# Performance work log

Hardware: AMD Instinct MI355X
Metric: run time of the kernel (lower is better)

## Reference

```python
import jax, jax.numpy as jnp
import numpy as np

NUM_BINS = 256          # CLAHE histogram bins (kornia default)
GRID = (8, 8)           # CLAHE tile grid (kornia default)
LOG_GAIN = 2.5          # module init arg
CLIP_LIMIT = 1.0        # module init arg


def normalize_in_range(x, lo=0.0, hi=1.0):
    mn = x.min()
    mx = x.max()
    return (x - mn) / (mx - mn) * (hi - lo) + lo


def adjust_log(x, gain):
    # skimage/kornia log adjust: gain * log2(1 + x)
    return gain * jnp.log2(1.0 + x)


def equalize_clahe(x, clip_limit=CLIP_LIMIT, grid=GRID):
    B, C, H, W = x.shape
    gh, gw = grid
    th = -(-H // gh)   # ceil tile height
    tw = -(-W // gw)   # ceil tile width
    Hp, Wp = th * gh, tw * gw
    if (Hp, Wp) != (H, W):
        x = jnp.pad(x, ((0, 0), (0, 0), (0, Hp - H), (0, Wp - W)), mode='reflect')

    # bin index per pixel (values saturated into [0,1])
    xc = jnp.clip(x, 0.0, 1.0)
    bins = jnp.clip((xc * NUM_BINS).astype(jnp.int32), 0, NUM_BINS - 1)  # B,C,Hp,Wp

    # --- per-tile histograms: (B*C*gh*gw) tiles of th*tw pixels ---
    tb = bins.reshape(B, C, gh, th, gw, tw).transpose(0, 1, 2, 4, 3, 5)
    tb = tb.reshape(B * C * gh * gw, th * tw)
    hist = jax.vmap(lambda ix: jnp.bincount(ix, length=NUM_BINS))(tb).astype(jnp.float32)

    pixels = th * tw
    # --- clip + uniform redistribution of excess ---
    if clip_limit > 0:
        clip_max = max(int(clip_limit * pixels // NUM_BINS), 1)
        excess = jnp.maximum(hist - clip_max, 0.0).sum(-1)
        hist = jnp.minimum(hist, float(clip_max))
        redist = jnp.floor(excess / NUM_BINS)
        residual = excess - redist * NUM_BINS
        hist = hist + redist[:, None] \
             + (jnp.arange(NUM_BINS)[None, :] < residual[:, None]).astype(hist.dtype)

    # --- CDF -> LUT in [0, 255] ---
    lut = jnp.clip(jnp.floor(jnp.cumsum(hist, -1) * ((NUM_BINS - 1) / pixels)), 0.0, NUM_BINS - 1.0)
    lut = lut.reshape(B, C, gh, gw, NUM_BINS)

    # --- bilinear interpolation between the 4 neighboring tile LUTs ---
    iy = jnp.arange(Hp, dtype=jnp.float32)
    ty = (iy + 0.5) / th - 0.5
    y0f = jnp.floor(ty)
    wy = (ty - y0f)[:, None]                                   # Hp x 1
    y0 = jnp.clip(y0f.astype(jnp.int32), 0, gh - 1)[:, None]
    y1 = jnp.clip(y0f.astype(jnp.int32) + 1, 0, gh - 1)[:, None]

    ix = jnp.arange(Wp, dtype=jnp.float32)
    tx = (ix + 0.5) / tw - 0.5
    x0f = jnp.floor(tx)
    wx = (tx - x0f)[None, :]
    x0 = jnp.clip(x0f.astype(jnp.int32), 0, gw - 1)[None, :]
    x1 = jnp.clip(x0f.astype(jnp.int32) + 1, 0, gw - 1)[None, :]

    flat_lut = lut.reshape(-1)
    bidx = jnp.arange(B)[:, None, None, None]
    cidx = jnp.arange(C)[None, :, None, None]

    def gather(yi, xi):
        idx = (((bidx * C + cidx) * gh + yi) * gw + xi) * NUM_BINS + bins
        return flat_lut[idx]

    v = (1.0 - wy) * ((1.0 - wx) * gather(y0, x0) + wx * gather(y0, x1)) \
        + wy * ((1.0 - wx) * gather(y1, x0) + wx * gather(y1, x1))
    out = v / (NUM_BINS - 1)
    return out[..., :H, :W]


def setup_inputs() -> dict:
    key = jax.random.key(0)
    x = jax.random.uniform(key, (8, 1, 2048, 2048), dtype=jnp.float32)
    return {"x": x}


def reference(x):
    shape = x.shape
    x = normalize_in_range(x, 0.0, 1.0)
    x = adjust_log(x, gain=LOG_GAIN)
    x = equalize_clahe(x, clip_limit=CLIP_LIMIT)
    x = normalize_in_range(x, 0.0, 1.0)
    return x.reshape(shape)
```

## Files before the change

### kernel.cpp

```cpp
#include <hip/hip_runtime.h>

#define NIMG 8
#define IMH 2048
#define IMW 2048
#define GH 8
#define GW 8
#define TH 256
#define TW 256
#define NBINS 256
#define NTPI 64
#define CLIP_MAXF 256.0f
#define LUT_SCALE 0.0038909912109375f
#define LOG_GAIN_F 2.5f

#define MM_BLOCKS 1024
#define APPLY_BLOCKS (16 * 16 * NIMG)

__device__ __forceinline__ int pix_bin(float v, float mn, float den) {
    float xn = (v - mn) / den;
    float t  = LOG_GAIN_F * log2f(1.0f + xn);
    float xc = fminf(fmaxf(t, 0.0f), 1.0f);
    int b = (int)(xc * 256.0f);
    return min(max(b, 0), 255);
}

__device__ __forceinline__ void mm4(float4 v, float& mn, float& mx) {
    mn = fminf(mn, fminf(fminf(v.x, v.y), fminf(v.z, v.w)));
    mx = fmaxf(mx, fmaxf(fmaxf(v.x, v.y), fmaxf(v.z, v.w)));
}

template <int NWAVES>
__device__ __forceinline__ void block_minmax(float& mn, float& mx, int t) {
#pragma unroll
    for (int m = 32; m >= 1; m >>= 1) {
        mn = fminf(mn, __shfl_xor(mn, m, 64));
        mx = fmaxf(mx, __shfl_xor(mx, m, 64));
    }
    __shared__ float smn[NWAVES], smx[NWAVES];
    int wid = t >> 6, lid = t & 63;
    if (lid == 0) { smn[wid] = mn; smx[wid] = mx; }
    __syncthreads();
    if (t == 0) {
#pragma unroll
        for (int i = 1; i < NWAVES; i++) { mn = fminf(mn, smn[i]); mx = fmaxf(mx, smx[i]); }
    }
}

__global__ __launch_bounds__(256) void k_minmax_in(const float4* __restrict__ x,
                                                   float2* __restrict__ red) {
    int t = threadIdx.x;
    size_t base = (size_t)blockIdx.x * 8192 + t;
    float mn = 3.4e38f, mx = -3.4e38f;
#pragma unroll
    for (int k = 0; k < 32; k += 4) {
        float4 v0 = x[base + (size_t)(k + 0) * 256];
        float4 v1 = x[base + (size_t)(k + 1) * 256];
        float4 v2 = x[base + (size_t)(k + 2) * 256];
        float4 v3 = x[base + (size_t)(k + 3) * 256];
        mm4(v0, mn, mx); mm4(v1, mn, mx); mm4(v2, mn, mx); mm4(v3, mn, mx);
    }
    block_minmax<4>(mn, mx, t);
    if (t == 0) red[blockIdx.x] = make_float2(mn, mx);
}

__global__ __launch_bounds__(256) void k_reduce_minmax(const float2* __restrict__ red, int n,
                                                       float* __restrict__ sc, int slot) {
    int t = threadIdx.x;
    float mn = 3.4e38f, mx = -3.4e38f;
    for (int i = t; i < n; i += 256) {
        float2 p = red[i];
        mn = fminf(mn, p.x);
        mx = fmaxf(mx, p.y);
    }
    block_minmax<4>(mn, mx, t);
    if (t == 0) { sc[slot] = mn; sc[slot + 1] = mx; }
}

template <bool STOREBINS>
__global__ __launch_bounds__(512) void k_hist(const float* __restrict__ x,
                                              const float* __restrict__ sc,
                                              float* __restrict__ hist,
                                              uchar4* __restrict__ bins) {
    __shared__ unsigned sh[NBINS];
    int t = threadIdx.x;
    if (t < NBINS) sh[t] = 0u;
    __syncthreads();

    int tile = blockIdx.x;
    int img  = blockIdx.y;
    int ty = tile >> 3, tx = tile & 7;
    float mn = sc[0], mx = sc[1];
    float den = mx - mn;

    size_t base = ((size_t)img * IMH + (size_t)ty * TH) * IMW + (size_t)tx * TW;
    const float* xt = x + base;
    int lid = t & 63;
    int rowoff = t >> 6;
    int c4 = t & 63;

    for (int it = 0; it < 32; ++it) {
        int r = (it << 3) + rowoff;
        float4 v = *(const float4*)(xt + (size_t)r * IMW + (c4 << 2));
        int b[4];
        b[0] = pix_bin(v.x, mn, den);
        b[1] = pix_bin(v.y, mn, den);
        b[2] = pix_bin(v.z, mn, den);
        b[3] = pix_bin(v.w, mn, den);
#pragma unroll
        for (int j = 0; j < 4; j++) {
            bool hot = (b[j] == 255);
            unsigned long long m = __ballot(hot);
            if (!hot) atomicAdd(&sh[b[j]], 1u);
            if (lid == 0 && m) atomicAdd(&sh[255], (unsigned)__popcll(m));
        }
        if (STOREBINS) {
            uchar4 q;
            q.x = (unsigned char)b[0]; q.y = (unsigned char)b[1];
            q.z = (unsigned char)b[2]; q.w = (unsigned char)b[3];
            bins[(base + (size_t)r * IMW + (size_t)(c4 << 2)) >> 2] = q;
        }
    }
    __syncthreads();
    if (t < NBINS)
        hist[((size_t)img * NTPI + tile) * NBINS + t] = (float)sh[t];
}

__global__ __launch_bounds__(256) void k_lut(const float* __restrict__ hist,
                                             float* __restrict__ lut) {
    int t = threadIdx.x;
    int tile = blockIdx.x;
    float h = hist[(size_t)tile * NBINS + t];
    float ex = fmaxf(h - CLIP_MAXF, 0.0f);

    float s = ex;
#pragma unroll
    for (int m = 1; m < 64; m <<= 1) s += __shfl_xor(s, m, 64);
    __shared__ float wpart[4];
    int wid = t >> 6, lid = t & 63;
    if (lid == 0) wpart[wid] = s;
    __syncthreads();
    float excess = wpart[0] + wpart[1] + wpart[2] + wpart[3];

    h = fminf(h, CLIP_MAXF);
    float redist   = floorf(excess * (1.0f / 256.0f));
    float residual = excess - redist * 256.0f;
    h = h + redist + (((float)t < residual) ? 1.0f : 0.0f);

    float c = h;
#pragma unroll
    for (int m = 1; m < 64; m <<= 1) {
        float o = __shfl_up(c, m, 64);
        if (lid >= m) c += o;
    }
    __shared__ float wsum[4];
    if (lid == 63) wsum[wid] = c;
    __syncthreads();
    float off = 0.0f;
    for (int i = 0; i < wid; i++) off += wsum[i];
    c += off;

    float l = fminf(floorf(c * LUT_SCALE), 255.0f);
    l = fmaxf(l, 0.0f);
    lut[(size_t)tile * NBINS + t] = l;
}

template <bool USE_BINS, bool FINAL>
__global__ __launch_bounds__(256) void k_apply(const uchar4* __restrict__ bins,
                                               const float* __restrict__ x,
                                               const float* __restrict__ lut,
                                               const float* __restrict__ sc,
                                               float2* __restrict__ red,
                                               float4* __restrict__ out) {
    __shared__ float L[4][NBINS];
    int t = threadIdx.x;
    int qx = blockIdx.x, qy = blockIdx.y, img = blockIdx.z;
    int ty = qy >> 1, tx = qx >> 1;
    int yA = (qy & 1) ? ty : max(ty - 1, 0);
    int yB = (qy & 1) ? min(ty + 1, GH - 1) : ty;
    int xA = (qx & 1) ? tx : max(tx - 1, 0);
    int xB = (qx & 1) ? min(tx + 1, GW - 1) : tx;

    const float* lb = lut + (size_t)img * NTPI * NBINS;
    L[0][t] = lb[(size_t)(yA * GW + xA) * NBINS + t];
    L[1][t] = lb[(size_t)(yA * GW + xB) * NBINS + t];
    L[2][t] = lb[(size_t)(yB * GW + xA) * NBINS + t];
    L[3][t] = lb[(size_t)(yB * GW + xB) * NBINS + t];
    __syncthreads();

    float mn = 0.f, den = 1.f;
    if (!USE_BINS) { mn = sc[0]; den = sc[1] - mn; }
    float pmn = 0.f, oscale = 1.f;
    if (FINAL) {
        float vmn = sc[2], vmx = sc[3];
        pmn = vmn * (1.0f / 255.0f);
        float pmx = vmx * (1.0f / 255.0f);
        oscale = 1.0f / (pmx - pmn);
    }

    float vmnl = 3.4e38f, vmxl = -3.4e38f;
    int gy0 = qy << 7, gx0 = qx << 7;
    int rowoff = t >> 5;
    int c4 = t & 31;

    for (int it = 0; it < 16; ++it) {
        int r = (it << 3) + rowoff;
        int iy = gy0 + r;
        int ix0 = gx0 + (c4 << 2);
        size_t pidx = ((size_t)img * IMH + iy) * IMW + ix0;

        int b[4];
        if (USE_BINS) {
            uchar4 q = bins[pidx >> 2];
            b[0] = q.x; b[1] = q.y; b[2] = q.z; b[3] = q.w;
        } else {
            float4 v = *(const float4*)(x + pidx);
            b[0] = pix_bin(v.x, mn, den);
            b[1] = pix_bin(v.y, mn, den);
            b[2] = pix_bin(v.z, mn, den);
            b[3] = pix_bin(v.w, mn, den);
        }

        float tyf = ((float)iy + 0.5f) * (1.0f / 256.0f) - 0.5f;
        float wy = tyf - floorf(tyf);
        float4 o;
        float* op = &o.x;
#pragma unroll
        for (int j = 0; j < 4; j++) {
            float txf = ((float)(ix0 + j) + 0.5f) * (1.0f / 256.0f) - 0.5f;
            float wx = txf - floorf(txf);
            float g00 = L[0][b[j]], g01 = L[1][b[j]];
            float g10 = L[2][b[j]], g11 = L[3][b[j]];
            float v = (1.0f - wy) * ((1.0f - wx) * g00 + wx * g01) +
                      wy * ((1.0f - wx) * g10 + wx * g11);
            if (FINAL) {
                float p = v * (1.0f / 255.0f);
                op[j] = (p - pmn) * oscale;
            } else {
                vmnl = fminf(vmnl, v);
                vmxl = fmaxf(vmxl, v);
            }
        }
        if (FINAL) out[pidx >> 2] = o;
    }

    if (!FINAL) {
        block_minmax<4>(vmnl, vmxl, t);
        if (t == 0) {
            int bid = (img * 16 + qy) * 16 + qx;
            red[bid] = make_float2(vmnl, vmxl);
        }
    }
}

extern "C" void kernel_launch(void* const* d_in, const int* in_sizes, int n_in,
                              void* d_out, int out_size, void* d_ws, size_t ws_size,
                              hipStream_t stream) {
    const float* x = (const float*)d_in[0];
    float4* out = (float4*)d_out;

    unsigned char* ws = (unsigned char*)d_ws;
    float* sc     = (float*)ws;
    float* hist   = (float*)(ws + 64);
    float* lut    = (float*)(ws + 64 + 512 * 1024);
    float2* red1  = (float2*)(ws + 64 + 1024 * 1024);
    float2* red2  = (float2*)(ws + 64 + 1024 * 1024 + 8192);
    uchar4* bins  = (uchar4*)(ws + 2 * 1024 * 1024);

    size_t need_bins = 2 * 1024 * 1024 + (size_t)NIMG * IMH * IMW;
    bool use_bins = (ws_size >= need_bins);

    k_minmax_in<<<dim3(MM_BLOCKS), dim3(256), 0, stream>>>((const float4*)x, red1);
    k_reduce_minmax<<<dim3(1), dim3(256), 0, stream>>>(red1, MM_BLOCKS, sc, 0);

    if (use_bins)
        k_hist<true><<<dim3(NTPI, NIMG), dim3(512), 0, stream>>>(x, sc, hist, bins);
    else
        k_hist<false><<<dim3(NTPI, NIMG), dim3(512), 0, stream>>>(x, sc, hist, bins);

    k_lut<<<dim3(NIMG * NTPI), dim3(256), 0, stream>>>(hist, lut);

    dim3 qgrid(16, 16, NIMG);
    if (use_bins) {
        k_apply<true, false><<<qgrid, dim3(256), 0, stream>>>(bins, x, lut, sc, red2, out);
        k_reduce_minmax<<<dim3(1), dim3(256), 0, stream>>>(red2, APPLY_BLOCKS, sc, 2);
        k_apply<true, true><<<qgrid, dim3(256), 0, stream>>>(bins, x, lut, sc, red2, out);
    } else {
        k_apply<false, false><<<qgrid, dim3(256), 0, stream>>>(bins, x, lut, sc, red2, out);
        k_reduce_minmax<<<dim3(1), dim3(256), 0, stream>>>(red2, APPLY_BLOCKS, sc, 2);
        k_apply<false, true><<<qgrid, dim3(256), 0, stream>>>(bins, x, lut, sc, red2, out);
    }
}
```

Before: 127.4 us.

## Fuse minmax reductions and LUT build into consumer kernels, cutting launches

The single-block min/max reduction kernels are removed. Each histogram block now reduces the 2048 partial min/max pairs itself, and each final apply block reduces the 2048 apply partials redundantly. The LUT clip and CDF computation moves into the histogram kernel, which now runs 1024 threads per tile, so the hist buffer and the separate LUT launch go away. This cuts kernel launches and serial tiny-kernel bubbles, in exchange for redundant reduction work in every block and larger blocks.

Result: faster. 121.4 us (-4.7%).

```diff
diff --git a/kernel.cpp b/kernel.cpp
--- a/kernel.cpp
+++ b/kernel.cpp
@@ -5,15 +5,13 @@
 #define IMW 2048
 #define GH 8
 #define GW 8
-#define TH 256
-#define TW 256
 #define NBINS 256
 #define NTPI 64
 #define CLIP_MAXF 256.0f
 #define LUT_SCALE 0.0038909912109375f
 #define LOG_GAIN_F 2.5f
 
-#define MM_BLOCKS 1024
+#define MM_BLOCKS 2048
 #define APPLY_BLOCKS (16 * 16 * NIMG)
 
 __device__ __forceinline__ int pix_bin(float v, float mn, float den) {
@@ -30,7 +28,7 @@
 }
 
 template <int NWAVES>
-__device__ __forceinline__ void block_minmax(float& mn, float& mx, int t) {
+__device__ __forceinline__ void block_minmax_all(float& mn, float& mx, int t) {
 #pragma unroll
     for (int m = 32; m >= 1; m >>= 1) {
         mn = fminf(mn, __shfl_xor(mn, m, 64));
@@ -40,26 +38,25 @@
     int wid = t >> 6, lid = t & 63;
     if (lid == 0) { smn[wid] = mn; smx[wid] = mx; }
     __syncthreads();
-    if (t == 0) {
-#pragma unroll
-        for (int i = 1; i < NWAVES; i++) { mn = fminf(mn, smn[i]); mx = fmaxf(mx, smx[i]); }
-    }
+    mn = smn[0]; mx = smx[0];
+#pragma unroll
+    for (int i = 1; i < NWAVES; i++) { mn = fminf(mn, smn[i]); mx = fmaxf(mx, smx[i]); }
 }
 
 __global__ __launch_bounds__(256) void k_minmax_in(const float4* __restrict__ x,
                                                    float2* __restrict__ red) {
     int t = threadIdx.x;
-    size_t base = (size_t)blockIdx.x * 8192 + t;
+    size_t base = (size_t)blockIdx.x * 4096 + t;
     float mn = 3.4e38f, mx = -3.4e38f;
 #pragma unroll
-    for (int k = 0; k < 32; k += 4) {
+    for (int k = 0; k < 16; k += 4) {
         float4 v0 = x[base + (size_t)(k + 0) * 256];
         float4 v1 = x[base + (size_t)(k + 1) * 256];
         float4 v2 = x[base + (size_t)(k + 2) * 256];
         float4 v3 = x[base + (size_t)(k + 3) * 256];
         mm4(v0, mn, mx); mm4(v1, mn, mx); mm4(v2, mn, mx); mm4(v3, mn, mx);
     }
-    block_minmax<4>(mn, mx, t);
+    block_minmax_all<4>(mn, mx, t);
     if (t == 0) red[blockIdx.x] = make_float2(mn, mx);
 }
 
@@ -72,34 +69,43 @@
         mn = fminf(mn, p.x);
         mx = fmaxf(mx, p.y);
     }
-    block_minmax<4>(mn, mx, t);
+    block_minmax_all<4>(mn, mx, t);
     if (t == 0) { sc[slot] = mn; sc[slot + 1] = mx; }
 }
 
 template <bool STOREBINS>
-__global__ __launch_bounds__(512) void k_hist(const float* __restrict__ x,
-                                              const float* __restrict__ sc,
-                                              float* __restrict__ hist,
-                                              uchar4* __restrict__ bins) {
+__global__ __launch_bounds__(1024) void k_hist(const float* __restrict__ x,
+                                               const float2* __restrict__ red1,
+                                               float* __restrict__ lut,
+                                               uchar4* __restrict__ bins) {
+    int t = threadIdx.x;
+
+    float mn, mx;
+    {
+        float2 p0 = red1[t];
+        float2 p1 = red1[t + 1024];
+        mn = fminf(p0.x, p1.x);
+        mx = fmaxf(p0.y, p1.y);
+        block_minmax_all<16>(mn, mx, t);
+    }
+    float den = mx - mn;
+
     __shared__ unsigned sh[NBINS];
-    int t = threadIdx.x;
     if (t < NBINS) sh[t] = 0u;
     __syncthreads();
 
     int tile = blockIdx.x;
     int img  = blockIdx.y;
     int ty = tile >> 3, tx = tile & 7;
-    float mn = sc[0], mx = sc[1];
-    float den = mx - mn;
-
-    size_t base = ((size_t)img * IMH + (size_t)ty * TH) * IMW + (size_t)tx * TW;
+
+    size_t base = ((size_t)img * IMH + (size_t)ty * 256) * IMW + (size_t)tx * 256;
     const float* xt = x + base;
     int lid = t & 63;
     int rowoff = t >> 6;
     int c4 = t & 63;
 
-    for (int it = 0; it < 32; ++it) {
-        int r = (it << 3) + rowoff;
+    for (int it = 0; it < 16; ++it) {
+        int r = (it << 4) + rowoff;
         float4 v = *(const float4*)(xt + (size_t)r * IMW + (c4 << 2));
         int b[4];
         b[0] = pix_bin(v.x, mn, den);
@@ -121,22 +127,17 @@
         }
     }
     __syncthreads();
-    if (t < NBINS)
-        hist[((size_t)img * NTPI + tile) * NBINS + t] = (float)sh[t];
-}
-
-__global__ __launch_bounds__(256) void k_lut(const float* __restrict__ hist,
-                                             float* __restrict__ lut) {
-    int t = threadIdx.x;
-    int tile = blockIdx.x;
-    float h = hist[(size_t)tile * NBINS + t];
-    float ex = fmaxf(h - CLIP_MAXF, 0.0f);
-
+
+    int wid = t >> 6;
+    float h = 0.0f, ex = 0.0f;
+    if (t < NBINS) {
+        h = (float)sh[t];
+        ex = fmaxf(h - CLIP_MAXF, 0.0f);
+    }
     float s = ex;
 #pragma unroll
     for (int m = 1; m < 64; m <<= 1) s += __shfl_xor(s, m, 64);
-    __shared__ float wpart[4];
-    int wid = t >> 6, lid = t & 63;
+    __shared__ float wpart[16];
     if (lid == 0) wpart[wid] = s;
     __syncthreads();
     float excess = wpart[0] + wpart[1] + wpart[2] + wpart[3];
@@ -152,16 +153,17 @@
         float o = __shfl_up(c, m, 64);
         if (lid >= m) c += o;
     }
-    __shared__ float wsum[4];
+    __shared__ float wsum[16];
     if (lid == 63) wsum[wid] = c;
     __syncthreads();
-    float off = 0.0f;
-    for (int i = 0; i < wid; i++) off += wsum[i];
-    c += off;
-
-    float l = fminf(floorf(c * LUT_SCALE), 255.0f);
-    l = fmaxf(l, 0.0f);
-    lut[(size_t)tile * NBINS + t] = l;
+    if (t < NBINS) {
+        float off = 0.0f;
+        for (int i = 0; i < wid; i++) off += wsum[i];
+        c += off;
+        float l = fminf(floorf(c * LUT_SCALE), 255.0f);
+        l = fmaxf(l, 0.0f);
+        lut[((size_t)img * NTPI + tile) * NBINS + t] = l;
+    }
 }
 
 template <bool USE_BINS, bool FINAL>
@@ -169,10 +171,26 @@
                                                const float* __restrict__ x,
                                                const float* __restrict__ lut,
                                                const float* __restrict__ sc,
-                                               float2* __restrict__ red,
+                                               float2* __restrict__ red2,
                                                float4* __restrict__ out) {
     __shared__ float L[4][NBINS];
     int t = threadIdx.x;
+
+    float pmn = 0.f, oscale = 1.f;
+    if (FINAL) {
+        float vmn = 3.4e38f, vmx = -3.4e38f;
+#pragma unroll
+        for (int k = 0; k < 8; k++) {
+            float2 p = red2[t + k * 256];
+            vmn = fminf(vmn, p.x);
+            vmx = fmaxf(vmx, p.y);
+        }
+        block_minmax_all<4>(vmn, vmx, t);
+        pmn = vmn * (1.0f / 255.0f);
+        float pmx = vmx * (1.0f / 255.0f);
+        oscale = 1.0f / (pmx - pmn);
+    }
+
     int qx = blockIdx.x, qy = blockIdx.y, img = blockIdx.z;
     int ty = qy >> 1, tx = qx >> 1;
     int yA = (qy & 1) ? ty : max(ty - 1, 0);
@@ -189,13 +207,6 @@
 
     float mn = 0.f, den = 1.f;
     if (!USE_BINS) { mn = sc[0]; den = sc[1] - mn; }
-    float pmn = 0.f, oscale = 1.f;
-    if (FINAL) {
-        float vmn = sc[2], vmx = sc[3];
-        pmn = vmn * (1.0f / 255.0f);
-        float pmx = vmx * (1.0f / 255.0f);
-        oscale = 1.0f / (pmx - pmn);
-    }
 
     float vmnl = 3.4e38f, vmxl = -3.4e38f;
     int gy0 = qy << 7, gx0 = qx << 7;
@@ -244,10 +255,10 @@
     }
 
     if (!FINAL) {
-        block_minmax<4>(vmnl, vmxl, t);
+        block_minmax_all<4>(vmnl, vmxl, t);
         if (t == 0) {
             int bid = (img * 16 + qy) * 16 + qx;
-            red[bid] = make_float2(vmnl, vmxl);
+            red2[bid] = make_float2(vmnl, vmxl);
         }
     }
 }
@@ -260,33 +271,25 @@
 
     unsigned char* ws = (unsigned char*)d_ws;
     float* sc     = (float*)ws;
-    float* hist   = (float*)(ws + 64);
-    float* lut    = (float*)(ws + 64 + 512 * 1024);
-    float2* red1  = (float2*)(ws + 64 + 1024 * 1024);
-    float2* red2  = (float2*)(ws + 64 + 1024 * 1024 + 8192);
-    uchar4* bins  = (uchar4*)(ws + 2 * 1024 * 1024);
-
-    size_t need_bins = 2 * 1024 * 1024 + (size_t)NIMG * IMH * IMW;
+    float* lut    = (float*)(ws + 64);
+    float2* red1  = (float2*)(ws + 64 + 512 * 1024);
+    float2* red2  = (float2*)(ws + 64 + 512 * 1024 + 16384);
+    uchar4* bins  = (uchar4*)(ws + 1024 * 1024);
+
+    size_t need_bins = 1024 * 1024 + (size_t)NIMG * IMH * IMW;
     bool use_bins = (ws_size >= need_bins);
 
     k_minmax_in<<<dim3(MM_BLOCKS), dim3(256), 0, stream>>>((const float4*)x, red1);
-    k_reduce_minmax<<<dim3(1), dim3(256), 0, stream>>>(red1, MM_BLOCKS, sc, 0);
-
-    if (use_bins)
-        k_hist<true><<<dim3(NTPI, NIMG), dim3(512), 0, stream>>>(x, sc, hist, bins);
-    else
-        k_hist<false><<<dim3(NTPI, NIMG), dim3(512), 0, stream>>>(x, sc, hist, bins);
-
-    k_lut<<<dim3(NIMG * NTPI), dim3(256), 0, stream>>>(hist, lut);
 
     dim3 qgrid(16, 16, NIMG);
     if (use_bins) {
+        k_hist<true><<<dim3(NTPI, NIMG), dim3(1024), 0, stream>>>(x, red1, lut, bins);
         k_apply<true, false><<<qgrid, dim3(256), 0, stream>>>(bins, x, lut, sc, red2, out);
-        k_reduce_minmax<<<dim3(1), dim3(256), 0, stream>>>(red2, APPLY_BLOCKS, sc, 2);
         k_apply<true, true><<<qgrid, dim3(256), 0, stream>>>(bins, x, lut, sc, red2, out);
     } else {
+        k_reduce_minmax<<<dim3(1), dim3(256), 0, stream>>>(red1, MM_BLOCKS, sc, 0);
+        k_hist<false><<<dim3(NTPI, NIMG), dim3(1024), 0, stream>>>(x, red1, lut, bins);
         k_apply<false, false><<<qgrid, dim3(256), 0, stream>>>(bins, x, lut, sc, red2, out);
-        k_reduce_minmax<<<dim3(1), dim3(256), 0, stream>>>(red2, APPLY_BLOCKS, sc, 2);
         k_apply<false, true><<<qgrid, dim3(256), 0, stream>>>(bins, x, lut, sc, red2, out);
     }
 }
```
